# Performance work log

Measured on AMD Instinct MI355X. Metric: run time of the kernel, lower is better.

## Reference

```python
import jax, jax.numpy as jnp
import numpy as np
from jax import lax

FEAT = 16; STRIDE = 16; IMG = 256; K = 30; POOL = 7
NMS_TH = 0.85; TEMP = 0.07; B = 32; CLIP_DIM = 1024; PROJ = 256; NA = 9

def _anchors():
    scales = [8.0, 16.0, 32.0]; ratios = [0.5, 1.0, 2.0]
    A = []
    for i in range(FEAT):
        for j in range(FEAT):
            xc = (j + 0.5) * STRIDE; yc = (i + 0.5) * STRIDE
            for s in scales:
                for r in ratios:
                    w = s * r ** 0.5; h = s / r ** 0.5
                    A.append([xc - w / 2, yc - h / 2, xc + w / 2, yc + h / 2])
    return jnp.asarray(np.array(A, dtype=np.float32))  # [2304,4]

def _decode(reg, anchors):
    wh = anchors[:, 2:] - anchors[:, :2]; ctr = anchors[:, :2] + 0.5 * wh
    cx = reg[..., 0] * wh[:, 0] + ctr[:, 0]; cy = reg[..., 1] * wh[:, 1] + ctr[:, 1]
    pw = jnp.exp(reg[..., 2]) * wh[:, 0]; ph = jnp.exp(reg[..., 3]) * wh[:, 1]
    b = jnp.stack([cx - 0.5 * pw, cy - 0.5 * ph, cx + 0.5 * pw, cy + 0.5 * ph], -1)
    b = jnp.clip(b, 0.0, 256.0)
    x1, y1, x2, y2 = b[..., 0], b[..., 1], b[..., 2], b[..., 3]
    x2 = jnp.where(x2 - x1 < 1, x1 + 1, x2)
    y2 = jnp.where(y2 - y1 < 1, y1 + 1, y2)
    return jnp.stack([x1, y1, x2, y2], -1)

def _nms_keep(b):  # [K,4], already sorted by score desc
    x1, y1, x2, y2 = b[:, 0], b[:, 1], b[:, 2], b[:, 3]
    area = (x2 - x1) * (y2 - y1)
    iw = jnp.clip(jnp.minimum(x2[:, None], x2[None]) - jnp.maximum(x1[:, None], x1[None]), 0)
    ih = jnp.clip(jnp.minimum(y2[:, None], y2[None]) - jnp.maximum(y1[:, None], y1[None]), 0)
    inter = iw * ih
    iou = inter / (area[:, None] + area[None] - inter)
    idx = jnp.arange(K)
    def body(i, keep):
        supp = (idx > i) & (iou[i] > NMS_TH) & keep[i]
        return keep & ~supp
    return lax.fori_loop(0, K, body, jnp.ones(K, bool))

def _roi_align_mean(feats, bidx, rois):
    # roi_align(output 7x7, spatial_scale=1/16, sampling_ratio=1) then mean over bins
    N = rois.shape[0]; _, C, H, W = feats.shape
    sc = 1.0 / STRIDE
    x1, y1 = rois[:, 0] * sc, rois[:, 1] * sc
    rw = jnp.maximum(rois[:, 2] * sc - x1, 1.0); rh = jnp.maximum(rois[:, 3] * sc - y1, 1.0)
    g = jnp.arange(POOL, dtype=feats.dtype) + 0.5
    xs = x1[:, None] + g[None] * (rw / POOL)[:, None]  # [N,7]
    ys = y1[:, None] + g[None] * (rh / POOL)[:, None]
    X = jnp.broadcast_to(xs[:, None, :], (N, POOL, POOL))
    Y = jnp.broadcast_to(ys[:, :, None], (N, POOL, POOL))
    ok = (Y > -1) & (Y < H) & (X > -1) & (X < W)
    Xc = jnp.clip(X, 0, W - 1); Yc = jnp.clip(Y, 0, H - 1)
    x0 = jnp.floor(Xc).astype(jnp.int32); y0 = jnp.floor(Yc).astype(jnp.int32)
    x1i = jnp.minimum(x0 + 1, W - 1); y1i = jnp.minimum(y0 + 1, H - 1)
    lx = Xc - x0; ly = Yc - y0; hx = 1 - lx; hy = 1 - ly
    bN = bidx[:, None, None]
    f00 = feats[bN, :, y0, x0]; f01 = feats[bN, :, y0, x1i]  # [N,7,7,C]
    f10 = feats[bN, :, y1i, x0]; f11 = feats[bN, :, y1i, x1i]
    v = ((hy * hx)[..., None] * f00 + (hy * lx)[..., None] * f01
         + (ly * hx)[..., None] * f10 + (ly * lx)[..., None] * f11)
    v = v * ok[..., None]
    return v.mean(axis=(1, 2))  # [N,C]

def _roi_labels(gt_masks, bidx, rois):
    g = gt_masks[:, 0]  # [B,256,256]
    I = jnp.pad(jnp.cumsum(jnp.cumsum(g, 1), 2), ((0, 0), (1, 0), (1, 0)))  # integral image
    c = jnp.clip(rois.astype(jnp.int32), 0, IMG)
    x1, y1, x2, y2 = c[:, 0], c[:, 1], c[:, 2], c[:, 3]
    s = I[bidx, y2, x2] - I[bidx, y1, x2] - I[bidx, y2, x1] + I[bidx, y1, x1]
    cnt = (y2 - y1) * (x2 - x1)
    return jnp.where(cnt > 0, s / jnp.maximum(cnt, 1) > 0.5, False)

def _supcon(proj, labels, valid):
    nf = proj / jnp.clip(jnp.linalg.norm(proj, axis=1, keepdims=True), 1e-12)
    sim = (nf @ nf.T) / TEMP
    N = proj.shape[0]
    nd = ~jnp.eye(N, dtype=bool)
    vv = valid[:, None] & valid[None]
    pos = (labels[:, None] == labels[None]) & nd & vv
    vmask = nd & vv
    es = jnp.exp(sim)
    ratio = (es * pos).sum(1) / ((es * vmask).sum(1) + 1e-12)
    l = -jnp.log(ratio + 1e-12)
    active = valid & (pos.sum(1) > 0)
    cnt = active.sum()
    return jnp.where(cnt > 0, (l * active).sum() / jnp.maximum(cnt, 1), 0.0)

def _forward(clip_features, gt_masks, conv_w, conv_b, cls_w, cls_b, reg_w, reg_b,
             proj_w1, proj_b1, proj_w2, proj_b2):
    Bn = clip_features.shape[1]
    spatial = jnp.transpose(clip_features[1:], (1, 2, 0)).reshape(Bn, CLIP_DIM, FEAT, FEAT)
    x = jax.nn.relu(lax.conv_general_dilated(
        spatial, conv_w, (1, 1), 'SAME',
        dimension_numbers=('NCHW', 'OIHW', 'NCHW')) + conv_b[None, :, None, None])
    cls = jnp.einsum('bchw,ac->bahw', x, cls_w) + cls_b[None, :, None, None]
    reg = jnp.einsum('bchw,ac->bahw', x, reg_w) + reg_b[None, :, None, None]
    reg_p = reg.reshape(Bn, NA, 4, FEAT, FEAT).transpose(0, 3, 4, 1, 2).reshape(Bn, -1, 4)
    cls_p = cls.transpose(0, 2, 3, 1).reshape(Bn, -1)
    boxes = _decode(reg_p, _anchors())  # [B,2304,4]
    scores = jax.nn.sigmoid(cls_p)
    _, top_i = lax.top_k(scores, K)
    top_boxes = jnp.take_along_axis(boxes, top_i[..., None], axis=1)  # [B,K,4]
    keep = jax.vmap(_nms_keep)(top_boxes)  # [B,K]
    rois = lax.stop_gradient(top_boxes.reshape(-1, 4))  # torch roi_align/labels don't backprop thru roi coords
    valid = keep.reshape(-1)
    bidx = jnp.repeat(jnp.arange(Bn), K)
    pooled = _roi_align_mean(spatial, bidx, rois)  # [N,1024]
    h = jax.nn.relu(pooled @ proj_w1.T + proj_b1)
    proj = h @ proj_w2.T + proj_b2  # [N,256]
    labels = _roi_labels(gt_masks, bidx, rois)
    return _supcon(proj, labels, valid)

def setup_inputs() -> dict:
    key = jax.random.key(0)
    ks = jax.random.split(key, 8)
    s = 0.02
    return {
        'clip_features': jax.random.normal(ks[0], (257, B, CLIP_DIM), jnp.float32),
        'gt_masks': (jax.random.uniform(ks[1], (B, 1, IMG, IMG)) > 0.5).astype(jnp.float32),
        'conv_w': jax.random.normal(ks[2], (512, CLIP_DIM, 3, 3)) * s,
        'conv_b': jnp.zeros((512,)),
        'cls_w': jax.random.normal(ks[3], (NA, 512)) * s,
        'cls_b': jnp.zeros((NA,)),
        'reg_w': jax.random.normal(ks[4], (NA * 4, 512)) * s,
        'reg_b': jnp.zeros((NA * 4,)),
        'proj_w1': jax.random.normal(ks[5], (PROJ, CLIP_DIM)) * s,
        'proj_b1': jnp.zeros((PROJ,)),
        'proj_w2': jax.random.normal(ks[6], (PROJ, PROJ)) * s,
        'proj_b2': jnp.zeros((PROJ,)),
    }

def reference(clip_features, gt_masks, conv_w, conv_b, cls_w, cls_b, reg_w, reg_b,
              proj_w1, proj_b1, proj_w2, proj_b2):
    return _forward(clip_features, gt_masks, conv_w, conv_b, cls_w, cls_b, reg_w, reg_b,
                    proj_w1, proj_b1, proj_w2, proj_b2)
```

## Files before the change

### kernel.cpp

```cpp
#include <hip/hip_runtime.h>
#include <hip/hip_bf16.h>
#include <math.h>

typedef unsigned short u16;
typedef unsigned int u32;
typedef _Float16 f16;
typedef _Float16 f16x8 __attribute__((ext_vector_type(8)));
typedef float f32x4 __attribute__((ext_vector_type(4)));

#define BATCH 32
#define CIN   1024
#define COUT  512
#define NPOS  8192
#define K9    9216
#define KHALF 4608
#define TOPK  30
#define NROI  960
#define POOLN 7
#define IMG   256

#define O_XP0  0ull
#define O_XP1  4194304ull
#define O_CH   8388608ull
#define O_CL   12582912ull
#define O_WH   16777216ull
#define O_WL   19136512ull
#define O_Z    21495808ull
#define O_HW   21496064ull
#define O_SC   21519104ull
#define O_RG   21592832ull
#define O_ROI  21887744ull
#define O_VAL  21891584ull
#define O_LAB  21892544ull
#define O_W1T  21893504ull
#define O_W2T  22155648ull
#define WS_FLOATS 22221184ull
#define O_PO   0ull
#define O_NF   1474560ull
#define O_PS   1720320ull

__device__ __forceinline__ void gl_lds16(const void* g, void* l) {
    __builtin_amdgcn_global_load_lds(
        (const __attribute__((address_space(1))) u32*)g,
        (__attribute__((address_space(3))) u32*)l,
        16, 0, 0);
}

__device__ inline void split16(float x, u16& h, u16& l) {
    f16 hv = (f16)x;
    f16 lv = (f16)(x - (float)hv);
    h = *(u16*)&hv;
    l = *(u16*)&lv;
}

#define NB_CLIP 8192
#define NB_W    2048
#define NB_Z    1
#define NB_HW   90
#define NB_W1T  1024
#define NB_W2T  256
__global__ __launch_bounds__(256)
void convert_all(const float* __restrict__ clip, const float* __restrict__ conv_w,
                 const float* __restrict__ cls_w, const float* __restrict__ reg_w,
                 const float* __restrict__ w1, const float* __restrict__ w2,
                 u16* __restrict__ CH, u16* __restrict__ CL,
                 u16* __restrict__ WH, u16* __restrict__ WL,
                 u16* __restrict__ Z, float* __restrict__ HW,
                 float* __restrict__ w1T, float* __restrict__ w2T) {
    __shared__ float wsh[2304];
    int bid = blockIdx.x, t = threadIdx.x;
    if (bid < NB_CLIP) {
        int tid = bid * 256 + t;
        int c4  = (tid & 255) * 4;
        int pos = (tid >> 8) & 255;
        int b   = tid >> 16;
        float4 v = *(const float4*)(clip + ((size_t)(1 + pos) * 32 + b) * 1024 + c4);
        float xs[4] = {v.x, v.y, v.z, v.w};
        ushort4 hh, ll;
        u16* hp = (u16*)&hh; u16* lp = (u16*)&ll;
#pragma unroll
        for (int q = 0; q < 4; ++q) split16(xs[q], hp[q], lp[q]);
        size_t o = ((size_t)(b * 256 + pos)) * 1024 + c4;
        *(ushort4*)(CH + o) = hh;
        *(ushort4*)(CL + o) = ll;
    } else if (bid < NB_CLIP + NB_W) {
        int bid2 = bid - NB_CLIP;
        int o = bid2 >> 2, cblk = bid2 & 3;
        const float* src = conv_w + (size_t)o * K9 + cblk * 2304;
        for (int i = t; i < 2304; i += 256) wsh[i] = src[i];
        __syncthreads();
#pragma unroll
        for (int p = 0; p < 9; ++p) {
            float x = wsh[t * 9 + p];
            u16 h, l;
            split16(x, h, l);
            size_t o2 = (size_t)o * K9 + p * 1024 + cblk * 256 + t;
            WH[o2] = h; WL[o2] = l;
        }
    } else if (bid < NB_CLIP + NB_W + NB_Z) {
        Z[t] = 0; Z[256 + t] = 0;
    } else if (bid < NB_CLIP + NB_W + NB_Z + NB_HW) {
        int tid2 = (bid - NB_CLIP - NB_W - NB_Z) * 256 + t;
        if (tid2 < 45 * 512) {
            int c = tid2 / 45, a = tid2 % 45;
            HW[tid2] = (a < 9) ? cls_w[a * 512 + c] : reg_w[(a - 9) * 512 + c];
        }
    } else if (bid < NB_CLIP + NB_W + NB_Z + NB_HW + NB_W1T) {
        int tid2 = (bid - NB_CLIP - NB_W - NB_Z - NB_HW) * 256 + t;
        int o = tid2 >> 10, c = tid2 & 1023;
        w1T[c * 256 + o] = w1[(size_t)o * 1024 + c];
    } else {
        int tid2 = (bid - NB_CLIP - NB_W - NB_Z - NB_HW - NB_W1T) * 256 + t;
        int o = tid2 >> 8, c = tid2 & 255;
        w2T[c * 256 + o] = w2[(size_t)o * 256 + c];
    }
}

__global__ __launch_bounds__(256, 2)
void conv_mfma(const u16* __restrict__ CH, const u16* __restrict__ CL,
               const u16* __restrict__ WH, const u16* __restrict__ WL,
               const u16* __restrict__ ZS,
               float* __restrict__ XP0, float* __restrict__ XP1) {
    __shared__ __align__(16) u16 Ah[8192];
    __shared__ __align__(16) u16 Al[8192];
    __shared__ __align__(16) u16 Bh[8192];
    __shared__ __align__(16) u16 Bl[8192];

    const int t = threadIdx.x;
    const int gid = blockIdx.x;
    const int nb = gid >> 7;
    const int g  = gid & 127;
    const int mb = g >> 1;
    const int ks = g & 1;
    const int ksOff = ks * KHALF;
    float* __restrict__ XP = ks ? XP1 : XP0;

    const int wave = t >> 6, lane = t & 63;

    int qA[2], siA[2], sjA[2], bA[2];
    const u16* srcBh[2];
    const u16* srcBl[2];
#pragma unroll
    for (int j = 0; j < 2; ++j) {
        int r = wave * 32 + j * 16 + (lane >> 2);
        int s = lane & 3;
        int q = s ^ ((r >> 1) & 3);
        qA[j] = q;
        int m = mb * 128 + r;
        bA[j] = m >> 8;
        int ij = m & 255;
        siA[j] = ij >> 4; sjA[j] = ij & 15;
        int o = nb * 128 + r;
        srcBh[j] = WH + (size_t)o * K9 + q * 8;
        srcBl[j] = WL + (size_t)o * K9 + q * 8;
    }

    const int wm = wave >> 1, wn = wave & 1;
    const int l16 = lane & 15, quad = lane >> 4;
    int offA[4], offB[4];
#pragma unroll
    for (int q = 0; q < 4; ++q) {
        int ar = wm * 64 + q * 16 + l16;
        offA[q] = ar * 32 + ((quad ^ ((ar >> 1) & 3)) << 3);
        int br = wn * 64 + q * 16 + l16;
        offB[q] = br * 32 + ((quad ^ ((br >> 1) & 3)) << 3);
    }

    f32x4 acc[4][4];
#pragma unroll
    for (int r = 0; r < 4; ++r)
#pragma unroll
        for (int c = 0; c < 4; ++c) acc[r][c] = (f32x4){0.f, 0.f, 0.f, 0.f};

    auto issue = [&](int it, int buf) {
        const int kg = ksOff + it * 32;
        const int p = kg >> 10;
        const int cb = kg & 1023;
        const int di = p / 3, dj = p - di * 3;
        const int base = buf << 12;
#pragma unroll
        for (int j = 0; j < 2; ++j) {
            int ii = siA[j] + di - 1, jj = sjA[j] + dj - 1;
            bool ok = ((unsigned)ii < 16u) && ((unsigned)jj < 16u);
            size_t aoff = ok ? ((((size_t)bA[j] << 8) + (size_t)(ii * 16 + jj)) << 10) + cb + qA[j] * 8
                             : 0;
            const u16* gah = ok ? CH + aoff : ZS;
            const u16* gal = ok ? CL + aoff : ZS;
            int lb = base + wave * 1024 + j * 512;
            gl_lds16(gah,           &Ah[lb]);
            gl_lds16(gal,           &Al[lb]);
            gl_lds16(srcBh[j] + kg, &Bh[lb]);
            gl_lds16(srcBl[j] + kg, &Bl[lb]);
        }
    };

    issue(0, 0);
    for (int it = 0; it < 144; ++it) {
        const int cur = it & 1;
        __syncthreads();
        if (it + 1 < 144) issue(it + 1, cur ^ 1);

        const int fb = cur << 12;
        f16x8 fah[4], fal[4], fbh[4], fbl[4];
#pragma unroll
        for (int x = 0; x < 4; ++x) {
            fah[x] = *(const f16x8*)&Ah[fb + offA[x]];
            fal[x] = *(const f16x8*)&Al[fb + offA[x]];
            fbh[x] = *(const f16x8*)&Bh[fb + offB[x]];
            fbl[x] = *(const f16x8*)&Bl[fb + offB[x]];
        }
#pragma unroll
        for (int tm = 0; tm < 4; ++tm)
#pragma unroll
            for (int tn = 0; tn < 4; ++tn) {
                acc[tm][tn] = __builtin_amdgcn_mfma_f32_16x16x32_f16(fal[tm], fbh[tn], acc[tm][tn], 0, 0, 0);
                acc[tm][tn] = __builtin_amdgcn_mfma_f32_16x16x32_f16(fah[tm], fbl[tn], acc[tm][tn], 0, 0, 0);
                acc[tm][tn] = __builtin_amdgcn_mfma_f32_16x16x32_f16(fah[tm], fbh[tn], acc[tm][tn], 0, 0, 0);
            }
    }

#pragma unroll
    for (int tm = 0; tm < 4; ++tm) {
        int mbase = mb * 128 + wm * 64 + tm * 16 + quad * 4;
#pragma unroll
        for (int tn = 0; tn < 4; ++tn) {
            int o = nb * 128 + wn * 64 + tn * 16 + l16;
#pragma unroll
            for (int r = 0; r < 4; ++r)
                XP[(size_t)(mbase + r) * COUT + o] = acc[tm][tn][r];
        }
    }
}

__global__ __launch_bounds__(64)
void heads_kernel(const float* __restrict__ XP0, const float* __restrict__ XP1,
                  const float* __restrict__ conv_b, const float* __restrict__ HW,
                  const float* __restrict__ cls_b, const float* __restrict__ reg_b,
                  float* __restrict__ scores, float* __restrict__ regs) {
    __shared__ float xs[512];
    int mm = blockIdx.x;
    int t = threadIdx.x;
#pragma unroll
    for (int q = 0; q < 8; ++q) {
        int c = t + 64 * q;
        xs[c] = fmaxf(XP0[(size_t)mm * COUT + c] + XP1[(size_t)mm * COUT + c] + conv_b[c], 0.f);
    }
    __syncthreads();
    if (t < 45) {
        float acc = (t < 9) ? cls_b[t] : reg_b[t - 9];
        for (int c = 0; c < 512; ++c) acc = fmaf(xs[c], HW[c * 45 + t], acc);
        int b = mm >> 8, cell = mm & 255;
        if (t < 9) {
            scores[(size_t)b * 2304 + cell * 9 + t] = 1.f / (1.f + expf(-acc));
        } else {
            int ch = t - 9;
            regs[((size_t)b * 2304 + cell * 9 + (ch >> 2)) * 4 + (ch & 3)] = acc;
        }
    }
}

__global__ __launch_bounds__(256)
void topk_nms(const float* __restrict__ scores, const float* __restrict__ regs,
              float* __restrict__ rois, float* __restrict__ valid) {
    __shared__ float sc[2304];
    __shared__ float wv[4];
    __shared__ int   wi[4];
    __shared__ int   sel[TOPK];
    __shared__ float bx[TOPK][4];
    __shared__ float iou[TOPK * TOPK];
    __shared__ float keepsh[TOPK];
    int b = blockIdx.x, t = threadIdx.x;
    for (int q = t; q < 2304; q += 256) sc[q] = scores[(size_t)b * 2304 + q];
    __syncthreads();

    for (int k = 0; k < TOPK; ++k) {
        float bv = -1e30f; int bi = 1 << 30;
#pragma unroll
        for (int q = 0; q < 9; ++q) {
            int idx = t * 9 + q;
            float v = sc[idx];
            if (v > bv || (v == bv && idx < bi)) { bv = v; bi = idx; }
        }
        for (int off = 32; off; off >>= 1) {
            float ov = __shfl_down(bv, off);
            int   oi = __shfl_down(bi, off);
            if (ov > bv || (ov == bv && oi < bi)) { bv = ov; bi = oi; }
        }
        int lane = t & 63, w = t >> 6;
        if (lane == 0) { wv[w] = bv; wi[w] = bi; }
        __syncthreads();
        if (t == 0) {
            float fv = wv[0]; int fi = wi[0];
            for (int q = 1; q < 4; ++q)
                if (wv[q] > fv || (wv[q] == fv && wi[q] < fi)) { fv = wv[q]; fi = wi[q]; }
            sel[k] = fi;
            sc[fi] = -1e38f;
        }
        __syncthreads();
    }

    if (t < TOPK) {
        int n = sel[t];
        int cell = n / 9, a = n % 9;
        int ci = cell >> 4, cj = cell & 15;
        int siid = a / 3, riid = a % 3;
        const double scl[3] = {8.0, 16.0, 32.0};
        const double rat[3] = {0.5, 1.0, 2.0};
        double s = scl[siid], r = rat[riid];
        double wD = s * sqrt(r), hD = s / sqrt(r);
        double xc = (cj + 0.5) * 16.0, yc = (ci + 0.5) * 16.0;
        float ax1 = (float)(xc - wD / 2), ay1 = (float)(yc - hD / 2);
        float ax2 = (float)(xc + wD / 2), ay2 = (float)(yc + hD / 2);
        float aw = ax2 - ax1, ah = ay2 - ay1;
        float ctrx = ax1 + 0.5f * aw, ctry = ay1 + 0.5f * ah;
        const float* rg = regs + ((size_t)b * 2304 + n) * 4;
        float cx = rg[0] * aw + ctrx;
        float cy = rg[1] * ah + ctry;
        float pw = expf(rg[2]) * aw;
        float ph = expf(rg[3]) * ah;
        float x1 = cx - 0.5f * pw, y1 = cy - 0.5f * ph;
        float x2 = cx + 0.5f * pw, y2 = cy + 0.5f * ph;
        x1 = fminf(fmaxf(x1, 0.f), 256.f);
        y1 = fminf(fmaxf(y1, 0.f), 256.f);
        x2 = fminf(fmaxf(x2, 0.f), 256.f);
        y2 = fminf(fmaxf(y2, 0.f), 256.f);
        if (x2 - x1 < 1.f) x2 = x1 + 1.f;
        if (y2 - y1 < 1.f) y2 = y1 + 1.f;
        bx[t][0] = x1; bx[t][1] = y1; bx[t][2] = x2; bx[t][3] = y2;
    }
    __syncthreads();
    if (t < TOPK * TOPK) {
        int ii = t / TOPK, jj = t % TOPK;
        float xi1 = bx[ii][0], yi1 = bx[ii][1], xi2 = bx[ii][2], yi2 = bx[ii][3];
        float xj1 = bx[jj][0], yj1 = bx[jj][1], xj2 = bx[jj][2], yj2 = bx[jj][3];
        float ai = (xi2 - xi1) * (yi2 - yi1), aj = (xj2 - xj1) * (yj2 - yj1);
        float iw = fmaxf(fminf(xi2, xj2) - fmaxf(xi1, xj1), 0.f);
        float ih = fmaxf(fminf(yi2, yj2) - fmaxf(yi1, yj1), 0.f);
        float inter = iw * ih;
        iou[t] = inter / (ai + aj - inter);
    }
    __syncthreads();
    if (t == 0) {
        bool keep[TOPK];
        for (int q = 0; q < TOPK; ++q) keep[q] = true;
        for (int iK = 0; iK < TOPK; ++iK) {
            if (!keep[iK]) continue;
            for (int jK = iK + 1; jK < TOPK; ++jK)
                if (keep[jK] && iou[iK * TOPK + jK] > 0.85f) keep[jK] = false;
        }
        for (int q = 0; q < TOPK; ++q) keepsh[q] = keep[q] ? 1.f : 0.f;
    }
    __syncthreads();
    if (t < TOPK) {
        int rr = b * TOPK + t;
        rois[rr * 4 + 0] = bx[t][0]; rois[rr * 4 + 1] = bx[t][1];
        rois[rr * 4 + 2] = bx[t][2]; rois[rr * 4 + 3] = bx[t][3];
        valid[rr] = keepsh[t];
    }
}

__global__ __launch_bounds__(256)
void align_img(const float* __restrict__ clip, const float* __restrict__ rois,
               float* __restrict__ pooled) {
    __shared__ float slice[16384];
    int bid = blockIdx.x;
    int b = bid >> 4, cg = bid & 15;
    int t = threadIdx.x;
    for (int idx = t; idx < 16384; idx += 256) {
        int p = idx >> 6, c = idx & 63;
        slice[idx] = clip[(size_t)(1 + p) * 32768 + (size_t)b * 1024 + cg * 64 + c];
    }
    __syncthreads();
    int wv = t >> 6;
    int ch = t & 63;
    for (int rp = 0; rp < 8; ++rp) {
        int rl = rp * 4 + wv;
        if (rl >= TOPK) continue;
        int r = b * TOPK + rl;
        float rx1 = rois[r * 4 + 0] * 0.0625f, ry1 = rois[r * 4 + 1] * 0.0625f;
        float rw = fmaxf(rois[r * 4 + 2] * 0.0625f - rx1, 1.f);
        float rh = fmaxf(rois[r * 4 + 3] * 0.0625f - ry1, 1.f);
        float sx = rw / (float)POOLN, sy = rh / (float)POOLN;
        float acc = 0.f;
        for (int py = 0; py < POOLN; ++py) {
            float Y = ry1 + ((float)py + 0.5f) * sy;
            for (int px = 0; px < POOLN; ++px) {
                float Xx = rx1 + ((float)px + 0.5f) * sx;
                bool ok = (Y > -1.f) && (Y < 16.f) && (Xx > -1.f) && (Xx < 16.f);
                if (!ok) continue;
                float Xc = fminf(fmaxf(Xx, 0.f), 15.f);
                float Yc = fminf(fmaxf(Y, 0.f), 15.f);
                int x0 = (int)floorf(Xc), y0 = (int)floorf(Yc);
                int x1i = min(x0 + 1, 15), y1i = min(y0 + 1, 15);
                float lx = Xc - (float)x0, ly = Yc - (float)y0;
                float hx = 1.f - lx, hy = 1.f - ly;
                float w00 = hy * hx, w01 = hy * lx, w10 = ly * hx, w11 = ly * lx;
                float f00 = slice[(y0 * 16 + x0) * 64 + ch];
                float f01 = slice[(y0 * 16 + x1i) * 64 + ch];
                float f10 = slice[(y1i * 16 + x0) * 64 + ch];
                float f11 = slice[(y1i * 16 + x1i) * 64 + ch];
                acc += w00 * f00 + w01 * f01 + w10 * f10 + w11 * f11;
            }
        }
        pooled[(size_t)r * 1024 + cg * 64 + ch] = acc / 49.f;
    }
}

__global__ __launch_bounds__(256)
void labels_k(const float* __restrict__ gt, const float* __restrict__ rois,
              float* __restrict__ labels) {
    __shared__ float red[4];
    int r = blockIdx.x, t = threadIdx.x;
    int b = r / TOPK;
    int x1 = min(max((int)rois[r * 4 + 0], 0), 256);
    int y1 = min(max((int)rois[r * 4 + 1], 0), 256);
    int x2 = min(max((int)rois[r * 4 + 2], 0), 256);
    int y2 = min(max((int)rois[r * 4 + 3], 0), 256);
    int cnt = (x2 - x1) * (y2 - y1);
    float s = 0.f;
    if (cnt > 0) {
        const float* g = gt + (size_t)b * (IMG * IMG);
        for (int yy = y1; yy < y2; ++yy) {
            const float* row = g + yy * IMG;
            for (int xx = x1 + t; xx < x2; xx += 256) s += row[xx];
        }
    }
    for (int off = 32; off; off >>= 1) s += __shfl_down(s, off);
    if ((t & 63) == 0) red[t >> 6] = s;
    __syncthreads();
    if (t == 0) {
        float tot = red[0] + red[1] + red[2] + red[3];
        labels[r] = (cnt > 0 && 2.f * tot > (float)cnt) ? 1.f : 0.f;
    }
}

__global__ __launch_bounds__(256)
void fc_norm(const float* __restrict__ pooled, const float* __restrict__ w1T,
             const float* __restrict__ b1, const float* __restrict__ w2T,
             const float* __restrict__ b2, float* __restrict__ nf) {
    __shared__ float rows[4][1024];
    __shared__ float hsh[4][256];
    __shared__ float red[4];
    int r0 = blockIdx.x * 4, t = threadIdx.x;
    for (int q = 0; q < 4; ++q)
        for (int c = t; c < 1024; c += 256)
            rows[q][c] = pooled[(size_t)(r0 + q) * 1024 + c];
    __syncthreads();
    {
        float bv = b1[t];
        float acc[4] = {bv, bv, bv, bv};
        for (int c = 0; c < 1024; ++c) {
            float wv = w1T[c * 256 + t];
#pragma unroll
            for (int q = 0; q < 4; ++q) acc[q] = fmaf(rows[q][c], wv, acc[q]);
        }
#pragma unroll
        for (int q = 0; q < 4; ++q) hsh[q][t] = fmaxf(acc[q], 0.f);
    }
    __syncthreads();
    float pr[4];
    {
        float bv = b2[t];
        float acc[4] = {bv, bv, bv, bv};
        for (int c = 0; c < 256; ++c) {
            float wv = w2T[c * 256 + t];
#pragma unroll
            for (int q = 0; q < 4; ++q) acc[q] = fmaf(hsh[q][c], wv, acc[q]);
        }
#pragma unroll
        for (int q = 0; q < 4; ++q) pr[q] = acc[q];
    }
    for (int q = 0; q < 4; ++q) {
        float v = pr[q];
        float ss = v * v;
        for (int off = 32; off; off >>= 1) ss += __shfl_down(ss, off);
        if ((t & 63) == 0) red[t >> 6] = ss;
        __syncthreads();
        float tot = red[0] + red[1] + red[2] + red[3];
        float denom = fmaxf(sqrtf(tot), 1e-12f);
        nf[(size_t)(r0 + q) * 256 + t] = v / denom;
        __syncthreads();
    }
}

__global__ __launch_bounds__(256)
void supcon_half(const float* __restrict__ nf, const float* __restrict__ labels,
                 const float* __restrict__ valid, float* __restrict__ PS) {
    __shared__ float my[256];
    __shared__ float labs[NROI], vals[NROI];
    __shared__ float wsa[4], wsp[4];
    __shared__ int wnp[4];
    int bid = blockIdx.x, t = threadIdx.x;
    int i = bid >> 1, half = bid & 1;
    my[t] = nf[(size_t)i * 256 + t];
    for (int q = t; q < NROI; q += 256) { labs[q] = labels[q]; vals[q] = valid[q]; }
    __syncthreads();
    float vi = vals[i], li = labs[i];
    float sum_all = 0.f, sum_pos = 0.f;
    int np = 0;
    int w = t >> 6, lane = t & 63;
    float4 my4 = ((const float4*)my)[lane];
    int j0 = half * 480, j1 = j0 + 480;
    if (vi > 0.5f) {
        for (int j = j0 + w; j < j1; j += 4) {
            float4 v4 = ((const float4*)(nf + (size_t)j * 256))[lane];
            float p = my4.x * v4.x;
            p = fmaf(my4.y, v4.y, p);
            p = fmaf(my4.z, v4.z, p);
            p = fmaf(my4.w, v4.w, p);
#pragma unroll
            for (int off = 32; off; off >>= 1) p += __shfl_xor(p, off);
            if (j != i && vals[j] > 0.5f) {
                float e = expf(p / 0.07f);
                sum_all += e;
                if (labs[j] == li) { sum_pos += e; np++; }
            }
        }
    }
    if (lane == 0) { wsa[w] = sum_all; wsp[w] = sum_pos; wnp[w] = np; }
    __syncthreads();
    if (t == 0) {
        float sa = wsa[0] + wsa[1] + wsa[2] + wsa[3];
        float sp = wsp[0] + wsp[1] + wsp[2] + wsp[3];
        int tnp = wnp[0] + wnp[1] + wnp[2] + wnp[3];
        PS[(size_t)i * 6 + half * 3 + 0] = sa;
        PS[(size_t)i * 6 + half * 3 + 1] = sp;
        PS[(size_t)i * 6 + half * 3 + 2] = (float)tnp;
    }
}

__global__ __launch_bounds__(256)
void final_reduce2(const float* __restrict__ PS, const float* __restrict__ valid,
                   float* __restrict__ out) {
    __shared__ float rl[4], ra[4];
    int t = threadIdx.x;
    float sl = 0.f, sc = 0.f;
    for (int i = t; i < NROI; i += 256) {
        float sa = PS[(size_t)i * 6 + 0] + PS[(size_t)i * 6 + 3];
        float sp = PS[(size_t)i * 6 + 1] + PS[(size_t)i * 6 + 4];
        float np = PS[(size_t)i * 6 + 2] + PS[(size_t)i * 6 + 5];
        bool active = (valid[i] > 0.5f) && (np > 0.5f);
        float ratio = sp / (sa + 1e-12f);
        float l = -logf(ratio + 1e-12f);
        sl += active ? l : 0.f;
        sc += active ? 1.f : 0.f;
    }
    for (int off = 32; off; off >>= 1) { sl += __shfl_down(sl, off); sc += __shfl_down(sc, off); }
    if ((t & 63) == 0) { rl[t >> 6] = sl; ra[t >> 6] = sc; }
    __syncthreads();
    if (t == 0) {
        float L = rl[0] + rl[1] + rl[2] + rl[3];
        float A = ra[0] + ra[1] + ra[2] + ra[3];
        out[0] = (A > 0.f) ? (L / fmaxf(A, 1.f)) : 0.f;
    }
}

extern "C" void kernel_launch(void* const* d_in, const int* in_sizes, int n_in,
                              void* d_out, int out_size, void* d_ws, size_t ws_size,
                              hipStream_t stream) {
    const float* clip   = (const float*)d_in[0];
    const float* gt     = (const float*)d_in[1];
    const float* conv_w = (const float*)d_in[2];
    const float* conv_b = (const float*)d_in[3];
    const float* cls_w  = (const float*)d_in[4];
    const float* cls_b  = (const float*)d_in[5];
    const float* reg_w  = (const float*)d_in[6];
    const float* reg_b  = (const float*)d_in[7];
    const float* w1     = (const float*)d_in[8];
    const float* b1     = (const float*)d_in[9];
    const float* w2     = (const float*)d_in[10];
    const float* b2     = (const float*)d_in[11];

    if (ws_size < WS_FLOATS * sizeof(float)) return;

    float* ws  = (float*)d_ws;
    float* XP0 = ws + O_XP0;
    float* XP1 = ws + O_XP1;
    u16*   CH  = (u16*)(ws + O_CH);
    u16*   CL  = (u16*)(ws + O_CL);
    u16*   WHp = (u16*)(ws + O_WH);
    u16*   WLp = (u16*)(ws + O_WL);
    u16*   ZS  = (u16*)(ws + O_Z);
    float* HW  = ws + O_HW;
    float* SC  = ws + O_SC;
    float* RG  = ws + O_RG;
    float* ROI = ws + O_ROI;
    float* VAL = ws + O_VAL;
    float* LAB = ws + O_LAB;
    float* W1T = ws + O_W1T;
    float* W2T = ws + O_W2T;
    float* PO  = ws + O_PO;
    float* NF  = ws + O_NF;
    float* PS  = ws + O_PS;

    convert_all<<<NB_CLIP + NB_W + NB_Z + NB_HW + NB_W1T + NB_W2T, 256, 0, stream>>>(
        clip, conv_w, cls_w, reg_w, w1, w2, CH, CL, WHp, WLp, ZS, HW, W1T, W2T);
    conv_mfma<<<512, 256, 0, stream>>>(CH, CL, WHp, WLp, ZS, XP0, XP1);
    heads_kernel<<<NPOS, 64, 0, stream>>>(XP0, XP1, conv_b, HW, cls_b, reg_b, SC, RG);
    topk_nms<<<BATCH, 256, 0, stream>>>(SC, RG, ROI, VAL);
    align_img<<<512, 256, 0, stream>>>(clip, ROI, PO);
    labels_k<<<NROI, 256, 0, stream>>>(gt, ROI, LAB);
    fc_norm<<<NROI / 4, 256, 0, stream>>>(PO, W1T, b1, W2T, b2, NF);
    supcon_half<<<2 * NROI, 256, 0, stream>>>(NF, LAB, VAL, PS);
    final_reduce2<<<1, 256, 0, stream>>>(PS, VAL, (float*)d_out);
}
```

Measured before the change: 692.4 us.

## Enlarge conv GEMM tile to 256x128 with 8 waves and interleaved prefetch

```diff
diff --git a/kernel.cpp b/kernel.cpp
--- a/kernel.cpp
+++ b/kernel.cpp
@@ -116,54 +116,69 @@
     }
 }
 
-__global__ __launch_bounds__(256, 2)
+__device__ __forceinline__ void mfma_row(f32x4* accRow, f16x8 fah, f16x8 fal,
+                                         const f16x8* fbh, const f16x8* fbl) {
+    __builtin_amdgcn_s_setprio(1);
+#pragma unroll
+    for (int tn = 0; tn < 4; ++tn) {
+        accRow[tn] = __builtin_amdgcn_mfma_f32_16x16x32_f16(fal, fbh[tn], accRow[tn], 0, 0, 0);
+        accRow[tn] = __builtin_amdgcn_mfma_f32_16x16x32_f16(fah, fbl[tn], accRow[tn], 0, 0, 0);
+        accRow[tn] = __builtin_amdgcn_mfma_f32_16x16x32_f16(fah, fbh[tn], accRow[tn], 0, 0, 0);
+    }
+    __builtin_amdgcn_s_setprio(0);
+}
+
+__global__ __launch_bounds__(512)
 void conv_mfma(const u16* __restrict__ CH, const u16* __restrict__ CL,
                const u16* __restrict__ WH, const u16* __restrict__ WL,
                const u16* __restrict__ ZS,
                float* __restrict__ XP0, float* __restrict__ XP1) {
-    __shared__ __align__(16) u16 Ah[8192];
-    __shared__ __align__(16) u16 Al[8192];
+    __shared__ __align__(16) u16 Ah[16384];
+    __shared__ __align__(16) u16 Al[16384];
     __shared__ __align__(16) u16 Bh[8192];
     __shared__ __align__(16) u16 Bl[8192];
 
     const int t = threadIdx.x;
     const int gid = blockIdx.x;
-    const int nb = gid >> 7;
-    const int g  = gid & 127;
-    const int mb = g >> 1;
-    const int ks = g & 1;
+    const int ks = gid & 1;
+    const int mb = (gid >> 1) & 31;
+    const int nb = gid >> 6;
     const int ksOff = ks * KHALF;
     float* __restrict__ XP = ks ? XP1 : XP0;
 
     const int wave = t >> 6, lane = t & 63;
 
     int qA[2], siA[2], sjA[2], bA[2];
-    const u16* srcBh[2];
-    const u16* srcBl[2];
 #pragma unroll
     for (int j = 0; j < 2; ++j) {
         int r = wave * 32 + j * 16 + (lane >> 2);
         int s = lane & 3;
-        int q = s ^ ((r >> 1) & 3);
-        qA[j] = q;
-        int m = mb * 128 + r;
+        qA[j] = s ^ ((r >> 1) & 3);
+        int m = mb * 256 + r;
         bA[j] = m >> 8;
         int ij = m & 255;
         siA[j] = ij >> 4; sjA[j] = ij & 15;
+    }
+    const u16* srcBh;
+    const u16* srcBl;
+    {
+        int r = wave * 16 + (lane >> 2);
+        int s = lane & 3;
+        int q = s ^ ((r >> 1) & 3);
         int o = nb * 128 + r;
-        srcBh[j] = WH + (size_t)o * K9 + q * 8;
-        srcBl[j] = WL + (size_t)o * K9 + q * 8;
+        srcBh = WH + (size_t)o * K9 + q * 8;
+        srcBl = WL + (size_t)o * K9 + q * 8;
     }
 
     const int wm = wave >> 1, wn = wave & 1;
     const int l16 = lane & 15, quad = lane >> 4;
     int offA[4], offB[4];
 #pragma unroll
-    for (int q = 0; q < 4; ++q) {
-        int ar = wm * 64 + q * 16 + l16;
-        offA[q] = ar * 32 + ((quad ^ ((ar >> 1) & 3)) << 3);
-        int br = wn * 64 + q * 16 + l16;
-        offB[q] = br * 32 + ((quad ^ ((br >> 1) & 3)) << 3);
+    for (int q4 = 0; q4 < 4; ++q4) {
+        int ar = wm * 64 + q4 * 16 + l16;
+        offA[q4] = ar * 32 + ((quad ^ ((ar >> 1) & 3)) << 3);
+        int br = wn * 64 + q4 * 16 + l16;
+        offB[q4] = br * 32 + ((quad ^ ((br >> 1) & 3)) << 3);
     }
 
     f32x4 acc[4][4];
@@ -172,56 +187,95 @@
 #pragma unroll
         for (int c = 0; c < 4; ++c) acc[r][c] = (f32x4){0.f, 0.f, 0.f, 0.f};
 
-    auto issue = [&](int it, int buf) {
-        const int kg = ksOff + it * 32;
-        const int p = kg >> 10;
-        const int cb = kg & 1023;
-        const int di = p / 3, dj = p - di * 3;
-        const int base = buf << 12;
-#pragma unroll
-        for (int j = 0; j < 2; ++j) {
-            int ii = siA[j] + di - 1, jj = sjA[j] + dj - 1;
-            bool ok = ((unsigned)ii < 16u) && ((unsigned)jj < 16u);
-            size_t aoff = ok ? ((((size_t)bA[j] << 8) + (size_t)(ii * 16 + jj)) << 10) + cb + qA[j] * 8
-                             : 0;
-            const u16* gah = ok ? CH + aoff : ZS;
-            const u16* gal = ok ? CL + aoff : ZS;
-            int lb = base + wave * 1024 + j * 512;
-            gl_lds16(gah,           &Ah[lb]);
-            gl_lds16(gal,           &Al[lb]);
-            gl_lds16(srcBh[j] + kg, &Bh[lb]);
-            gl_lds16(srcBl[j] + kg, &Bl[lb]);
-        }
+    auto stageB = [&](int step, int buf) {
+        int kg = ksOff + step * 32;
+        int lb = buf * 4096 + wave * 512;
+        gl_lds16(srcBh + kg, &Bh[lb]);
+        gl_lds16(srcBl + kg, &Bl[lb]);
     };
-
-    issue(0, 0);
-    for (int it = 0; it < 144; ++it) {
+    auto stageA = [&](int step, int buf, int j) {
+        int kg = ksOff + step * 32;
+        int p = kg >> 10, cb = kg & 1023;
+        int di = p / 3, dj = p - di * 3;
+        int ii = siA[j] + di - 1, jj = sjA[j] + dj - 1;
+        bool ok = ((unsigned)ii < 16u) && ((unsigned)jj < 16u);
+        size_t aoff = ((((size_t)bA[j] << 8) + (size_t)(ii * 16 + jj)) << 10) + cb + qA[j] * 8;
+        const u16* gah = ok ? CH + aoff : ZS;
+        const u16* gal = ok ? CL + aoff : ZS;
+        int lb = buf * 8192 + wave * 1024 + j * 512;
+        gl_lds16(gah, &Ah[lb]);
+        gl_lds16(gal, &Al[lb]);
+    };
+
+    stageB(0, 0);
+    stageA(0, 0, 0);
+    stageA(0, 0, 1);
+
+    for (int it = 0; it < 143; ++it) {
         const int cur = it & 1;
-        __syncthreads();
-        if (it + 1 < 144) issue(it + 1, cur ^ 1);
-
-        const int fb = cur << 12;
-        f16x8 fah[4], fal[4], fbh[4], fbl[4];
-#pragma unroll
-        for (int x = 0; x < 4; ++x) {
-            fah[x] = *(const f16x8*)&Ah[fb + offA[x]];
-            fal[x] = *(const f16x8*)&Al[fb + offA[x]];
-            fbh[x] = *(const f16x8*)&Bh[fb + offB[x]];
-            fbl[x] = *(const f16x8*)&Bl[fb + offB[x]];
-        }
-#pragma unroll
-        for (int tm = 0; tm < 4; ++tm)
-#pragma unroll
-            for (int tn = 0; tn < 4; ++tn) {
-                acc[tm][tn] = __builtin_amdgcn_mfma_f32_16x16x32_f16(fal[tm], fbh[tn], acc[tm][tn], 0, 0, 0);
-                acc[tm][tn] = __builtin_amdgcn_mfma_f32_16x16x32_f16(fah[tm], fbl[tn], acc[tm][tn], 0, 0, 0);
-                acc[tm][tn] = __builtin_amdgcn_mfma_f32_16x16x32_f16(fah[tm], fbh[tn], acc[tm][tn], 0, 0, 0);
-            }
+        const int nxt = cur ^ 1;
+        const int fa  = cur << 13;
+        const int fbB = cur << 12;
+
+        f16x8 fbh[4], fbl[4];
+
+        stageB(it + 1, nxt);
+        asm volatile("s_waitcnt vmcnt(2)" ::: "memory");
+        __builtin_amdgcn_s_barrier();
+        __builtin_amdgcn_sched_barrier(0);
+#pragma unroll
+        for (int q4 = 0; q4 < 4; ++q4) {
+            fbh[q4] = *(const f16x8*)&Bh[fbB + offB[q4]];
+            fbl[q4] = *(const f16x8*)&Bl[fbB + offB[q4]];
+        }
+        {
+            f16x8 fah = *(const f16x8*)&Ah[fa + offA[0]];
+            f16x8 fal = *(const f16x8*)&Al[fa + offA[0]];
+            mfma_row(acc[0], fah, fal, fbh, fbl);
+        }
+        stageA(it + 1, nxt, 0);
+        {
+            f16x8 fah = *(const f16x8*)&Ah[fa + offA[1]];
+            f16x8 fal = *(const f16x8*)&Al[fa + offA[1]];
+            mfma_row(acc[1], fah, fal, fbh, fbl);
+        }
+        stageA(it + 1, nxt, 1);
+        {
+            f16x8 fah = *(const f16x8*)&Ah[fa + offA[2]];
+            f16x8 fal = *(const f16x8*)&Al[fa + offA[2]];
+            mfma_row(acc[2], fah, fal, fbh, fbl);
+        }
+        {
+            f16x8 fah = *(const f16x8*)&Ah[fa + offA[3]];
+            f16x8 fal = *(const f16x8*)&Al[fa + offA[3]];
+            mfma_row(acc[3], fah, fal, fbh, fbl);
+        }
+        __builtin_amdgcn_s_barrier();
+        __builtin_amdgcn_sched_barrier(0);
+    }
+
+    {
+        const int fa = 8192, fbB = 4096;
+        f16x8 fbh[4], fbl[4];
+        asm volatile("s_waitcnt vmcnt(0)" ::: "memory");
+        __builtin_amdgcn_s_barrier();
+        __builtin_amdgcn_sched_barrier(0);
+#pragma unroll
+        for (int q4 = 0; q4 < 4; ++q4) {
+            fbh[q4] = *(const f16x8*)&Bh[fbB + offB[q4]];
+            fbl[q4] = *(const f16x8*)&Bl[fbB + offB[q4]];
+        }
+#pragma unroll
+        for (int tm = 0; tm < 4; ++tm) {
+            f16x8 fah = *(const f16x8*)&Ah[fa + offA[tm]];
+            f16x8 fal = *(const f16x8*)&Al[fa + offA[tm]];
+            mfma_row(acc[tm], fah, fal, fbh, fbl);
+        }
     }
 
 #pragma unroll
     for (int tm = 0; tm < 4; ++tm) {
-        int mbase = mb * 128 + wm * 64 + tm * 16 + quad * 4;
+        int mbase = mb * 256 + wm * 64 + tm * 16 + quad * 4;
 #pragma unroll
         for (int tn = 0; tn < 4; ++tn) {
             int o = nb * 128 + wn * 64 + tn * 16 + l16;
@@ -595,7 +649,7 @@
 
     convert_all<<<NB_CLIP + NB_W + NB_Z + NB_HW + NB_W1T + NB_W2T, 256, 0, stream>>>(
         clip, conv_w, cls_w, reg_w, w1, w2, CH, CL, WHp, WLp, ZS, HW, W1T, W2T);
-    conv_mfma<<<512, 256, 0, stream>>>(CH, CL, WHp, WLp, ZS, XP0, XP1);
+    conv_mfma<<<256, 512, 0, stream>>>(CH, CL, WHp, WLp, ZS, XP0, XP1);
     heads_kernel<<<NPOS, 64, 0, stream>>>(XP0, XP1, conv_b, HW, cls_b, reg_b, SC, RG);
     topk_nms<<<BATCH, 256, 0, stream>>>(SC, RG, ROI, VAL);
     align_img<<<512, 256, 0, stream>>>(clip, ROI, PO);
```

Result: slower. 710.5 us (+2.6%).

## Tile supervised-contrastive similarity into 32x64 blocks with LDS reuse

Applied to the files above, without the earlier changes.

```diff
diff --git a/kernel.cpp b/kernel.cpp
--- a/kernel.cpp
+++ b/kernel.cpp
@@ -18,6 +18,7 @@
 #define NROI  960
 #define POOLN 7
 #define IMG   256
+#define SJT   15
 
 #define O_XP0  0ull
 #define O_XP1  4194304ull
@@ -484,48 +485,72 @@
 }
 
 __global__ __launch_bounds__(256)
-void supcon_half(const float* __restrict__ nf, const float* __restrict__ labels,
+void supcon_tile(const float* __restrict__ nf, const float* __restrict__ labels,
                  const float* __restrict__ valid, float* __restrict__ PS) {
-    __shared__ float my[256];
-    __shared__ float labs[NROI], vals[NROI];
-    __shared__ float wsa[4], wsp[4];
-    __shared__ int wnp[4];
-    int bid = blockIdx.x, t = threadIdx.x;
-    int i = bid >> 1, half = bid & 1;
-    my[t] = nf[(size_t)i * 256 + t];
-    for (int q = t; q < NROI; q += 256) { labs[q] = labels[q]; vals[q] = valid[q]; }
-    __syncthreads();
-    float vi = vals[i], li = labs[i];
-    float sum_all = 0.f, sum_pos = 0.f;
-    int np = 0;
+    __shared__ __align__(16) float nfT[64 * 256];
+    __shared__ __align__(16) float myl[32 * 256];
+    __shared__ float labj[64], valj[64];
+    int bid = blockIdx.x;
+    int it = bid / SJT, jt = bid - it * SJT;
+    int i0 = it * 32, j0 = jt * 64;
+    int t = threadIdx.x;
+
+    for (int idx = t; idx < 64 * 256; idx += 256) {
+        int j = idx >> 8, c = idx & 255;
+        float v = nf[(size_t)(j0 + j) * 256 + c];
+        int byte_off = ((j << 10) + (c << 2)) ^ ((j & 7) << 4);
+        *(float*)((char*)nfT + byte_off) = v;
+    }
+    for (int idx = t; idx < 32 * 256; idx += 256)
+        myl[idx] = nf[(size_t)i0 * 256 + idx];
+    if (t < 64) { labj[t] = labels[j0 + t]; valj[t] = valid[j0 + t]; }
+    __syncthreads();
+
     int w = t >> 6, lane = t & 63;
-    float4 my4 = ((const float4*)my)[lane];
-    int j0 = half * 480, j1 = j0 + 480;
-    if (vi > 0.5f) {
-        for (int j = j0 + w; j < j1; j += 4) {
-            float4 v4 = ((const float4*)(nf + (size_t)j * 256))[lane];
-            float p = my4.x * v4.x;
-            p = fmaf(my4.y, v4.y, p);
-            p = fmaf(my4.z, v4.z, p);
-            p = fmaf(my4.w, v4.w, p);
-#pragma unroll
-            for (int off = 32; off; off >>= 1) p += __shfl_xor(p, off);
-            if (j != i && vals[j] > 0.5f) {
-                float e = expf(p / 0.07f);
-                sum_all += e;
-                if (labs[j] == li) { sum_pos += e; np++; }
-            }
-        }
-    }
-    if (lane == 0) { wsa[w] = sum_all; wsp[w] = sum_pos; wnp[w] = np; }
-    __syncthreads();
-    if (t == 0) {
-        float sa = wsa[0] + wsa[1] + wsa[2] + wsa[3];
-        float sp = wsp[0] + wsp[1] + wsp[2] + wsp[3];
-        int tnp = wnp[0] + wnp[1] + wnp[2] + wnp[3];
-        PS[(size_t)i * 6 + half * 3 + 0] = sa;
-        PS[(size_t)i * 6 + half * 3 + 1] = sp;
-        PS[(size_t)i * 6 + half * 3 + 2] = (float)tnp;
+    const char* jrow = (const char*)nfT + (lane << 10);
+    const int sw = (lane & 7) << 4;
+    const float* my0 = &myl[(w * 8) * 256];
+
+    float d[8];
+#pragma unroll
+    for (int q = 0; q < 8; ++q) d[q] = 0.f;
+    for (int c = 0; c < 256; c += 4) {
+        float4 b4 = *(const float4*)(jrow + ((c << 2) ^ sw));
+#pragma unroll
+        for (int q = 0; q < 8; ++q) {
+            float4 a4 = *(const float4*)(my0 + q * 256 + c);
+            d[q] = fmaf(a4.x, b4.x, d[q]);
+            d[q] = fmaf(a4.y, b4.y, d[q]);
+            d[q] = fmaf(a4.z, b4.z, d[q]);
+            d[q] = fmaf(a4.w, b4.w, d[q]);
+        }
+    }
+
+    int jg = j0 + lane;
+    float vj = valj[lane], lj = labj[lane];
+#pragma unroll
+    for (int q = 0; q < 8; ++q) {
+        int ig = i0 + w * 8 + q;
+        float vi = valid[ig];
+        float li = labels[ig];
+        bool vmask = (vi > 0.5f) && (vj > 0.5f) && (jg != ig);
+        float e  = vmask ? expf(d[q] / 0.07f) : 0.f;
+        bool pos = vmask && (lj == li);
+        float ep  = pos ? e : 0.f;
+        float npv = pos ? 1.f : 0.f;
+        float sa = e, sp = ep, sn = npv;
+#pragma unroll
+        for (int off = 32; off; off >>= 1) {
+            sa += __shfl_xor(sa, off);
+            sp += __shfl_xor(sp, off);
+            sn += __shfl_xor(sn, off);
+        }
+        if (lane == 0) {
+            size_t o = ((size_t)ig * SJT + jt) * 3;
+            PS[o + 0] = sa;
+            PS[o + 1] = sp;
+            PS[o + 2] = sn;
+        }
     }
 }
 
@@ -536,9 +561,13 @@
     int t = threadIdx.x;
     float sl = 0.f, sc = 0.f;
     for (int i = t; i < NROI; i += 256) {
-        float sa = PS[(size_t)i * 6 + 0] + PS[(size_t)i * 6 + 3];
-        float sp = PS[(size_t)i * 6 + 1] + PS[(size_t)i * 6 + 4];
-        float np = PS[(size_t)i * 6 + 2] + PS[(size_t)i * 6 + 5];
+        float sa = 0.f, sp = 0.f, np = 0.f;
+        for (int jt = 0; jt < SJT; ++jt) {
+            size_t o = ((size_t)i * SJT + jt) * 3;
+            sa += PS[o + 0];
+            sp += PS[o + 1];
+            np += PS[o + 2];
+        }
         bool active = (valid[i] > 0.5f) && (np > 0.5f);
         float ratio = sp / (sa + 1e-12f);
         float l = -logf(ratio + 1e-12f);
@@ -601,6 +630,6 @@
     align_img<<<512, 256, 0, stream>>>(clip, ROI, PO);
     labels_k<<<NROI, 256, 0, stream>>>(gt, ROI, LAB);
     fc_norm<<<NROI / 4, 256, 0, stream>>>(PO, W1T, b1, W2T, b2, NF);
-    supcon_half<<<2 * NROI, 256, 0, stream>>>(NF, LAB, VAL, PS);
+    supcon_tile<<<30 * SJT, 256, 0, stream>>>(NF, LAB, VAL, PS);
     final_reduce2<<<1, 256, 0, stream>>>(PS, VAL, (float*)d_out);
 }
```

New measurement: 649.5 us. 1.07x faster.
